# Kernel optimization log

Measured on AMD Instinct MI355X. Metric: run time of the kernel, lower is better.

The kernel has to match this reference:

```python
import jax, jax.numpy as jnp
import numpy as np

N = 50000      # nodes
E = 200000     # edges (before self-loops)
HID = 64       # hidden_channels
HEADS = 8
VOCAB = 100    # node-type vocabulary for the embedding
NEG_SLOPE = 0.2
EPS = 1e-16


def _gatv2(x, src, dst, Wl, bl, Wr, br, att, bias, heads, out_ch):
    """GATv2Conv (PyG defaults: share_weights=False, concat=True, neg_slope=0.2).
    x: [N, F_in]; src/dst: [E_tot] (self-loops already appended).
    Returns [N, heads*out_ch]."""
    n = x.shape[0]
    xl = (x @ Wl + bl).reshape(n, heads, out_ch)   # source transform
    xr = (x @ Wr + br).reshape(n, heads, out_ch)   # target transform
    m = xl[src] + xr[dst]                          # [E, H, C]
    e = jnp.einsum('ehc,hc->eh', jax.nn.leaky_relu(m, NEG_SLOPE), att)  # [E, H]
    # segment softmax over incoming edges of each destination node
    e_max = jax.ops.segment_max(e, dst, num_segments=n)
    e_exp = jnp.exp(e - e_max[dst])
    denom = jax.ops.segment_sum(e_exp, dst, num_segments=n)
    alpha = e_exp / (denom[dst] + EPS)             # [E, H]
    out = jax.ops.segment_sum(alpha[:, :, None] * xl[src], dst, num_segments=n)
    return out.reshape(n, heads * out_ch) + bias


def setup_inputs() -> dict:
    key = jax.random.key(0)
    ks = jax.random.split(key, 16)
    s = 0.1
    return {
        'x': jax.random.randint(ks[0], (N,), 0, VOCAB),
        'edge_index': jax.random.randint(ks[1], (2, E), 0, N),
        'emb': jax.random.normal(ks[2], (VOCAB, HID), dtype=jnp.float32) * s,
        'Wl1': jax.random.normal(ks[3], (HID, HEADS * HID), dtype=jnp.float32) * s,
        'bl1': jnp.zeros((HEADS * HID,), jnp.float32),
        'Wr1': jax.random.normal(ks[4], (HID, HEADS * HID), dtype=jnp.float32) * s,
        'br1': jnp.zeros((HEADS * HID,), jnp.float32),
        'att1': jax.random.normal(ks[5], (HEADS, HID), dtype=jnp.float32) * s,
        'bias1': jnp.zeros((HEADS * HID,), jnp.float32),
        'Wl2': jax.random.normal(ks[6], (HEADS * HID, 2), dtype=jnp.float32) * s,
        'bl2': jnp.zeros((2,), jnp.float32),
        'Wr2': jax.random.normal(ks[7], (HEADS * HID, 2), dtype=jnp.float32) * s,
        'br2': jnp.zeros((2,), jnp.float32),
        'att2': jax.random.normal(ks[8], (1, 2), dtype=jnp.float32) * s,
        'bias2': jnp.zeros((2,), jnp.float32),
    }


def reference(x, edge_index, emb, Wl1, bl1, Wr1, br1, att1, bias1,
              Wl2, bl2, Wr2, br2, att2, bias2):
    # PyG GATv2Conv adds self-loops by default
    loops = jnp.arange(N, dtype=edge_index.dtype)
    src = jnp.concatenate([edge_index[0], loops])
    dst = jnp.concatenate([edge_index[1], loops])

    h = emb[x]                                       # embedding lookup [N, HID]
    # dropout layers are identity in eval mode
    h = _gatv2(h, src, dst, Wl1, bl1, Wr1, br1, att1, bias1, HEADS, HID)
    h = jax.nn.elu(h)
    out = _gatv2(h, src, dst, Wl2, bl2, Wr2, br2, att2, bias2, 1, 2)
    return out                                       # [N, 2]
```

## Files before the change

kernel.cpp:

```cpp
#include <hip/hip_runtime.h>
#include <hip/hip_fp16.h>
#include <math.h>

#define NEG_SLOPE 0.2f
#define EPSV 1e-16f
#define CAP 32
#define MAXV 100
#define NBLK 256

struct __align__(16) h8v { __half2 a, b, c, d; };

__global__ __launch_bounds__(256) void kA_tables_fill(
    const float* __restrict__ emb, const float* __restrict__ Wl1,
    const float* __restrict__ bl1, const float* __restrict__ Wr1,
    const float* __restrict__ br1,
    const int* __restrict__ srcE, const int* __restrict__ dstE,
    const int* __restrict__ x,
    float* __restrict__ table_l, float* __restrict__ table_r,
    __half* __restrict__ table_lh,
    int* __restrict__ cnt, int* __restrict__ adj,
    int nb_tab, int nb_E, int E, int N, int VOCAB, int tshift)
{
    int b = blockIdx.x;
    if (b < nb_tab) {
        int idx = b * 256 + threadIdx.x;
        if (idx < VOCAB * 512) {
            int t = idx >> 9, o = idx & 511;
            float sl = bl1[o], sr = br1[o];
            const float* e = emb + t * 64;
            #pragma unroll 8
            for (int k = 0; k < 64; ++k) {
                float ev = e[k];
                sl = fmaf(ev, Wl1[k * 512 + o], sl);
                sr = fmaf(ev, Wr1[k * 512 + o], sr);
            }
            table_l[idx] = sl;
            table_r[idx] = sr;
            table_lh[idx] = __float2half_rn(sl);
        }
    } else if (b < nb_tab + nb_E) {
        int e = (b - nb_tab) * 256 + threadIdx.x;
        if (e < E) {
            int d = dstE[e];
            int sv = srcE[e];
            int pos = 1 + atomicAdd(&cnt[d], 1);
            if (pos < CAP) adj[d * CAP + pos] = (sv << tshift) | x[sv];
        }
    } else {
        int d = (b - nb_tab - nb_E) * 256 + threadIdx.x;
        if (d < N) adj[d * CAP] = (d << tshift) | x[d];
    }
}

__global__ __launch_bounds__(256) void kB_epair(
    const float* __restrict__ table_l, const float* __restrict__ table_r,
    const float* __restrict__ att1, float* __restrict__ exp_pair, int VOCAB)
{
    int idx = blockIdx.x * 256 + threadIdx.x;
    if (idx >= VOCAB * VOCAB * 8) return;
    int h = idx & 7;
    int p = idx >> 3;
    int ts = p % VOCAB;
    int td = p / VOCAB;
    const float4* tl = (const float4*)(table_l + ts * 512 + h * 64);
    const float4* tr = (const float4*)(table_r + td * 512 + h * 64);
    const float4* a  = (const float4*)(att1 + h * 64);
    float s = 0.f;
    #pragma unroll
    for (int c4 = 0; c4 < 16; ++c4) {
        float4 l = tl[c4], r = tr[c4], av = a[c4];
        float m0 = l.x + r.x; m0 = m0 > 0.f ? m0 : NEG_SLOPE * m0; s = fmaf(m0, av.x, s);
        float m1 = l.y + r.y; m1 = m1 > 0.f ? m1 : NEG_SLOPE * m1; s = fmaf(m1, av.y, s);
        float m2 = l.z + r.z; m2 = m2 > 0.f ? m2 : NEG_SLOPE * m2; s = fmaf(m2, av.z, s);
        float m3 = l.w + r.w; m3 = m3 > 0.f ? m3 : NEG_SLOPE * m3; s = fmaf(m3, av.w, s);
    }
    exp_pair[idx] = __expf(s);
}

__global__ __launch_bounds__(1024, 1) void k4_node_agg(
    const int* __restrict__ x, const int* __restrict__ cnt,
    const int* __restrict__ adj,
    const __half* __restrict__ table_lh, const float* __restrict__ exp_pair,
    const float* __restrict__ bias1,
    const float* __restrict__ Wl2, const float* __restrict__ bl2,
    const float* __restrict__ Wr2, const float* __restrict__ br2,
    float2* __restrict__ xl2, float2* __restrict__ xr2,
    int N, int VOCAB, int tmask)
{
    __shared__ __half tab[MAXV * 512];
    int vcap = min(VOCAB, MAXV);
    {
        const int4* sp = (const int4*)table_lh;
        int4* tp = (int4*)tab;
        for (int i = threadIdx.x; i < vcap * 64; i += 1024) tp[i] = sp[i];
    }
    __syncthreads();

    int lane = threadIdx.x & 63;
    int wv = threadIdx.x >> 6;
    int hc = lane >> 3;

    int chunk = (N + (int)gridDim.x - 1) / (int)gridDim.x;
    int nd1 = min((int)(blockIdx.x + 1) * chunk, N);

    const float4* b4 = (const float4*)(bias1 + lane * 8);
    float4 b0 = b4[0], b1 = b4[1];
    float bb[8] = {b0.x, b0.y, b0.z, b0.w, b1.x, b1.y, b1.z, b1.w};
    const float4* wl4 = (const float4*)(Wl2 + lane * 16);
    const float4* wr4 = (const float4*)(Wr2 + lane * 16);

    for (int d0 = blockIdx.x * chunk + wv; d0 < nd1; d0 += 16) {
        int wid = __builtin_amdgcn_readfirstlane(d0);
        const int* arow = adj + wid * CAP;
        int4 A0 = ((const int4*)arow)[0];
        int4 A1 = ((const int4*)arow)[1];
        int deg = min(cnt[wid], CAP - 1) + 1;
        int td = x[wid];
        const float* ep = exp_pair + (size_t)td * (VOCAB * 8);

        int ts[8];
        ts[0] = A0.x & tmask; ts[1] = A0.y & tmask;
        ts[2] = A0.z & tmask; ts[3] = A0.w & tmask;
        ts[4] = A1.x & tmask; ts[5] = A1.y & tmask;
        ts[6] = A1.z & tmask; ts[7] = A1.w & tmask;
        #pragma unroll
        for (int e = 1; e < 8; ++e) if (e >= deg) ts[e] = ts[0];

        float sw = 0.f;
        float acc[8] = {0.f, 0.f, 0.f, 0.f, 0.f, 0.f, 0.f, 0.f};

        {
            float we[4];
            #pragma unroll
            for (int e = 0; e < 4; ++e) we[e] = ep[ts[e] * 8 + hc];
            h8v hv[4];
            #pragma unroll
            for (int e = 0; e < 4; ++e)
                hv[e] = *(const h8v*)(tab + ts[e] * 512 + lane * 8);
            #pragma unroll
            for (int e = 0; e < 4; ++e) {
                float w = (e < deg) ? we[e] : 0.f;
                sw += w;
                float2 p0 = __half22float2(hv[e].a);
                float2 p1 = __half22float2(hv[e].b);
                float2 p2 = __half22float2(hv[e].c);
                float2 p3 = __half22float2(hv[e].d);
                acc[0] = fmaf(w, p0.x, acc[0]); acc[1] = fmaf(w, p0.y, acc[1]);
                acc[2] = fmaf(w, p1.x, acc[2]); acc[3] = fmaf(w, p1.y, acc[3]);
                acc[4] = fmaf(w, p2.x, acc[4]); acc[5] = fmaf(w, p2.y, acc[5]);
                acc[6] = fmaf(w, p3.x, acc[6]); acc[7] = fmaf(w, p3.y, acc[7]);
            }
        }
        if (deg > 4) {
            float we[4];
            #pragma unroll
            for (int e = 0; e < 4; ++e) we[e] = ep[ts[4 + e] * 8 + hc];
            h8v hv[4];
            #pragma unroll
            for (int e = 0; e < 4; ++e)
                hv[e] = *(const h8v*)(tab + ts[4 + e] * 512 + lane * 8);
            #pragma unroll
            for (int e = 0; e < 4; ++e) {
                float w = (4 + e < deg) ? we[e] : 0.f;
                sw += w;
                float2 p0 = __half22float2(hv[e].a);
                float2 p1 = __half22float2(hv[e].b);
                float2 p2 = __half22float2(hv[e].c);
                float2 p3 = __half22float2(hv[e].d);
                acc[0] = fmaf(w, p0.x, acc[0]); acc[1] = fmaf(w, p0.y, acc[1]);
                acc[2] = fmaf(w, p1.x, acc[2]); acc[3] = fmaf(w, p1.y, acc[3]);
                acc[4] = fmaf(w, p2.x, acc[4]); acc[5] = fmaf(w, p2.y, acc[5]);
                acc[6] = fmaf(w, p3.x, acc[6]); acc[7] = fmaf(w, p3.y, acc[7]);
            }
        }
        if (deg > 8) {
            for (int base = 8; base < deg; base += 4) {
                int t4i[4];
                #pragma unroll
                for (int u = 0; u < 4; ++u) {
                    int e = base + u;
                    t4i[u] = ((e < deg) ? arow[e] : arow[0]) & tmask;
                }
                float w4[4];
                #pragma unroll
                for (int u = 0; u < 4; ++u) w4[u] = ep[t4i[u] * 8 + hc];
                h8v g4[4];
                #pragma unroll
                for (int u = 0; u < 4; ++u)
                    g4[u] = *(const h8v*)(tab + t4i[u] * 512 + lane * 8);
                #pragma unroll
                for (int u = 0; u < 4; ++u) {
                    float w = (base + u < deg) ? w4[u] : 0.f;
                    sw += w;
                    float2 p0 = __half22float2(g4[u].a);
                    float2 p1 = __half22float2(g4[u].b);
                    float2 p2 = __half22float2(g4[u].c);
                    float2 p3 = __half22float2(g4[u].d);
                    acc[0] = fmaf(w, p0.x, acc[0]); acc[1] = fmaf(w, p0.y, acc[1]);
                    acc[2] = fmaf(w, p1.x, acc[2]); acc[3] = fmaf(w, p1.y, acc[3]);
                    acc[4] = fmaf(w, p2.x, acc[4]); acc[5] = fmaf(w, p2.y, acc[5]);
                    acc[6] = fmaf(w, p3.x, acc[6]); acc[7] = fmaf(w, p3.y, acc[7]);
                }
            }
        }
        float inv_dn = 1.f / (sw + EPSV);

        float h1[8];
        #pragma unroll
        for (int j = 0; j < 8; ++j) {
            float v = fmaf(acc[j], inv_dn, bb[j]);
            h1[j] = v > 0.f ? v : (__expf(v) - 1.f);
        }
        float sl0 = 0.f, sl1 = 0.f, sr0 = 0.f, sr1 = 0.f;
        #pragma unroll
        for (int k = 0; k < 4; ++k) {
            float4 vl = wl4[k], vr = wr4[k];
            float ha = h1[2 * k], hb = h1[2 * k + 1];
            sl0 = fmaf(ha, vl.x, sl0); sl1 = fmaf(ha, vl.y, sl1);
            sl0 = fmaf(hb, vl.z, sl0); sl1 = fmaf(hb, vl.w, sl1);
            sr0 = fmaf(ha, vr.x, sr0); sr1 = fmaf(ha, vr.y, sr1);
            sr0 = fmaf(hb, vr.z, sr0); sr1 = fmaf(hb, vr.w, sr1);
        }
        #pragma unroll
        for (int mm = 1; mm < 64; mm <<= 1) {
            sl0 += __shfl_xor(sl0, mm);
            sl1 += __shfl_xor(sl1, mm);
            sr0 += __shfl_xor(sr0, mm);
            sr1 += __shfl_xor(sr1, mm);
        }
        if (lane == 0) {
            xl2[wid] = make_float2(sl0 + bl2[0], sl1 + bl2[1]);
            xr2[wid] = make_float2(sr0 + br2[0], sr1 + br2[1]);
        }
    }
}

__global__ __launch_bounds__(256) void k5_layer2(
    const int* __restrict__ cnt, const int* __restrict__ adj,
    const float2* __restrict__ xl2, const float2* __restrict__ xr2,
    const float* __restrict__ att2, const float* __restrict__ bias2,
    float2* __restrict__ out, int N, int tshift)
{
    int wid = blockIdx.x * 4 + (threadIdx.x >> 6);
    int lane = threadIdx.x & 63;
    int g = lane >> 3, j = lane & 7;
    int d = wid * 8 + g;
    int dc = min(d, N - 1);
    int start = dc * CAP;
    float a0 = att2[0], a1 = att2[1];

    int aw = adj[start + j];
    int deg = min(cnt[dc], CAP - 1) + 1;
    float2 xr = xr2[dc];
    int src = min(aw >> tshift, N - 1);
    float2 xl = xl2[src];
    float m0 = xl.x + xr.x; m0 = m0 > 0.f ? m0 : NEG_SLOPE * m0;
    float m1 = xl.y + xr.y; m1 = m1 > 0.f ? m1 : NEG_SLOPE * m1;
    float ev = fmaf(a0, m0, a1 * m1);
    float w = (j < deg) ? __expf(ev) : 0.f;
    float s = w, o0 = w * xl.x, o1 = w * xl.y;

    for (int e = j + 8; e < deg; e += 8) {
        int src2 = min(adj[start + e] >> tshift, N - 1);
        float2 x2 = xl2[src2];
        float n0 = x2.x + xr.x; n0 = n0 > 0.f ? n0 : NEG_SLOPE * n0;
        float n1 = x2.y + xr.y; n1 = n1 > 0.f ? n1 : NEG_SLOPE * n1;
        float e2 = fmaf(a0, n0, a1 * n1);
        float w2 = __expf(e2);
        s += w2;
        o0 = fmaf(w2, x2.x, o0);
        o1 = fmaf(w2, x2.y, o1);
    }
    #pragma unroll
    for (int off = 1; off < 8; off <<= 1) {
        s  += __shfl_xor(s, off);
        o0 += __shfl_xor(o0, off);
        o1 += __shfl_xor(o1, off);
    }
    if (d < N && j == 0) {
        float inv = 1.f / (s + EPSV);
        out[d] = make_float2(fmaf(o0, inv, bias2[0]), fmaf(o1, inv, bias2[1]));
    }
}

extern "C" void kernel_launch(void* const* d_in, const int* in_sizes, int n_in,
                              void* d_out, int out_size, void* d_ws, size_t ws_size,
                              hipStream_t stream) {
    (void)n_in; (void)out_size; (void)ws_size;
    const int*   x     = (const int*)d_in[0];
    const int*   ei    = (const int*)d_in[1];
    const float* emb   = (const float*)d_in[2];
    const float* Wl1   = (const float*)d_in[3];
    const float* bl1   = (const float*)d_in[4];
    const float* Wr1   = (const float*)d_in[5];
    const float* br1   = (const float*)d_in[6];
    const float* att1  = (const float*)d_in[7];
    const float* bias1 = (const float*)d_in[8];
    const float* Wl2   = (const float*)d_in[9];
    const float* bl2   = (const float*)d_in[10];
    const float* Wr2   = (const float*)d_in[11];
    const float* br2   = (const float*)d_in[12];
    const float* att2  = (const float*)d_in[13];
    const float* bias2 = (const float*)d_in[14];
    float* out = (float*)d_out;

    int N = in_sizes[0];
    int E = in_sizes[1] / 2;
    int VOCAB = in_sizes[2] / 64;
    const int* srcE = ei;
    const int* dstE = ei + E;

    int tshift = 1;
    while ((1 << tshift) < VOCAB) ++tshift;
    int tmask = (1 << tshift) - 1;

    float*  table_l  = (float*)d_ws;
    float*  table_r  = table_l + (size_t)VOCAB * 512;
    float*  exp_pair = table_r + (size_t)VOCAB * 512;
    __half* table_lh = (__half*)(exp_pair + (size_t)VOCAB * VOCAB * 8);
    int*    cnt      = (int*)(table_lh + (size_t)VOCAB * 512);
    int*    adj      = cnt + ((N + 3) & ~3);
    float*  xl2      = (float*)(adj + (size_t)N * CAP);
    float*  xr2      = xl2 + 2 * (size_t)N;

    hipMemsetAsync(cnt, 0, sizeof(int) * (size_t)N, stream);

    int nb_tab = (VOCAB * 512 + 255) / 256;
    int nb_E = (E + 255) / 256;
    int nb_N = (N + 255) / 256;

    kA_tables_fill<<<nb_tab + nb_E + nb_N, 256, 0, stream>>>(
        emb, Wl1, bl1, Wr1, br1, srcE, dstE, x,
        table_l, table_r, table_lh, cnt, adj, nb_tab, nb_E, E, N, VOCAB, tshift);

    int nb_ep = (VOCAB * VOCAB * 8 + 255) / 256;
    kB_epair<<<nb_ep, 256, 0, stream>>>(table_l, table_r, att1, exp_pair, VOCAB);

    k4_node_agg<<<NBLK, 1024, 0, stream>>>(
        x, cnt, adj, table_lh, exp_pair, bias1, Wl2, bl2, Wr2, br2,
        (float2*)xl2, (float2*)xr2, N, VOCAB, tmask);

    k5_layer2<<<(N + 31) / 32, 256, 0, stream>>>(
        cnt, adj, (const float2*)xl2, (const float2*)xr2,
        att2, bias2, (float2*)out, N, tshift);
}
```

Baseline: 149.8 us.

## Prefetch per-destination exp row into LDS asynchronously and store exp pairs in fp16

The exp-pair table is now stored in half precision. Each wave copies the row for its destination type (800 halves) into a per-wave LDS buffer with global_load_lds. The copy for the next node is issued while the current node is still aggregating, and that node's adjacency and degree are also loaded one iteration ahead. Weight gathers come from LDS instead of scattered global reads, which hides gather latency. In exchange, shared memory use goes up, ordering relies on hand-placed waitcnt instructions, and the attention weights lose precision.

```diff
diff --git a/kernel.cpp b/kernel.cpp
--- a/kernel.cpp
+++ b/kernel.cpp
@@ -9,6 +9,12 @@
 #define NBLK 256
 
 struct __align__(16) h8v { __half2 a, b, c, d; };
+
+typedef __attribute__((address_space(1))) const unsigned int* gas1_t;
+typedef __attribute__((address_space(3))) unsigned int* las3_t;
+__device__ __forceinline__ void cp16_g2l(const void* g, void* l) {
+    __builtin_amdgcn_global_load_lds((gas1_t)g, (las3_t)l, 16, 0, 0);
+}
 
 __global__ __launch_bounds__(256) void kA_tables_fill(
     const float* __restrict__ emb, const float* __restrict__ Wl1,
@@ -54,7 +60,7 @@
 
 __global__ __launch_bounds__(256) void kB_epair(
     const float* __restrict__ table_l, const float* __restrict__ table_r,
-    const float* __restrict__ att1, float* __restrict__ exp_pair, int VOCAB)
+    const float* __restrict__ att1, __half* __restrict__ exph, int VOCAB)
 {
     int idx = blockIdx.x * 256 + threadIdx.x;
     if (idx >= VOCAB * VOCAB * 8) return;
@@ -74,13 +80,13 @@
         float m2 = l.z + r.z; m2 = m2 > 0.f ? m2 : NEG_SLOPE * m2; s = fmaf(m2, av.z, s);
         float m3 = l.w + r.w; m3 = m3 > 0.f ? m3 : NEG_SLOPE * m3; s = fmaf(m3, av.w, s);
     }
-    exp_pair[idx] = __expf(s);
+    exph[idx] = __float2half_rn(__expf(s));
 }
 
 __global__ __launch_bounds__(1024, 1) void k4_node_agg(
     const int* __restrict__ x, const int* __restrict__ cnt,
     const int* __restrict__ adj,
-    const __half* __restrict__ table_lh, const float* __restrict__ exp_pair,
+    const __half* __restrict__ table_lh, const __half* __restrict__ exph,
     const float* __restrict__ bias1,
     const float* __restrict__ Wl2, const float* __restrict__ bl2,
     const float* __restrict__ Wr2, const float* __restrict__ br2,
@@ -88,6 +94,7 @@
     int N, int VOCAB, int tmask)
 {
     __shared__ __half tab[MAXV * 512];
+    __shared__ __half eprow[16][800];
     int vcap = min(VOCAB, MAXV);
     {
         const int4* sp = (const int4*)table_lh;
@@ -100,23 +107,41 @@
     int wv = threadIdx.x >> 6;
     int hc = lane >> 3;
 
-    int chunk = (N + (int)gridDim.x - 1) / (int)gridDim.x;
-    int nd1 = min((int)(blockIdx.x + 1) * chunk, N);
-
-    const float4* b4 = (const float4*)(bias1 + lane * 8);
-    float4 b0 = b4[0], b1 = b4[1];
-    float bb[8] = {b0.x, b0.y, b0.z, b0.w, b1.x, b1.y, b1.z, b1.w};
+    int chunk = (N + NBLK - 1) / NBLK;
+    int b0 = blockIdx.x * chunk;
+    int nd1 = min(b0 + chunk, N);
+    int d0 = b0 + wv;
+    if (d0 >= nd1) return;
+
+    const float4* bp4 = (const float4*)(bias1 + lane * 8);
+    float4 bv0 = bp4[0], bv1 = bp4[1];
+    float bb[8] = {bv0.x, bv0.y, bv0.z, bv0.w, bv1.x, bv1.y, bv1.z, bv1.w};
     const float4* wl4 = (const float4*)(Wl2 + lane * 16);
     const float4* wr4 = (const float4*)(Wr2 + lane * 16);
 
-    for (int d0 = blockIdx.x * chunk + wv; d0 < nd1; d0 += 16) {
-        int wid = __builtin_amdgcn_readfirstlane(d0);
-        const int* arow = adj + wid * CAP;
-        int4 A0 = ((const int4*)arow)[0];
-        int4 A1 = ((const int4*)arow)[1];
-        int deg = min(cnt[wid], CAP - 1) + 1;
-        int td = x[wid];
-        const float* ep = exp_pair + (size_t)td * (VOCAB * 8);
+    __half* myrow = &eprow[wv][0];
+    const char* glane1 = (const char*)nullptr;
+
+    int tdC = x[d0];
+    {
+        const char* g = (const char*)(exph + (size_t)tdC * (VOCAB * 8));
+        cp16_g2l(g + lane * 16, (void*)myrow);
+        if (lane < 36)
+            cp16_g2l(g + 1024 + lane * 16, (void*)((char*)myrow + 1024));
+    }
+    int dn_seed = d0 + 16; if (dn_seed >= nd1) dn_seed = d0;
+    int tdN = x[dn_seed];
+    const int* arC = adj + d0 * CAP;
+    int4 A0 = ((const int4*)arC)[0];
+    int4 A1 = ((const int4*)arC)[1];
+    int degC = min(cnt[d0], CAP - 1) + 1;
+
+    for (int d = d0; d < nd1; d += 16) {
+        int dnext = d + 16;
+        bool hasN = dnext < nd1;
+        int dn1 = hasN ? dnext : d;
+        int dn2 = d + 32; if (dn2 >= nd1) dn2 = dn1;
+        const int* arow = adj + d * CAP;
 
         int ts[8];
         ts[0] = A0.x & tmask; ts[1] = A0.y & tmask;
@@ -124,73 +149,43 @@
         ts[4] = A1.x & tmask; ts[5] = A1.y & tmask;
         ts[6] = A1.z & tmask; ts[7] = A1.w & tmask;
         #pragma unroll
-        for (int e = 1; e < 8; ++e) if (e >= deg) ts[e] = ts[0];
+        for (int e = 1; e < 8; ++e) if (e >= degC) ts[e] = ts[0];
+
+        asm volatile("s_waitcnt vmcnt(0)" ::: "memory");
+
+        float we[8];
+        #pragma unroll
+        for (int e = 0; e < 4; ++e) we[e] = __half2float(myrow[ts[e] * 8 + hc]);
+        if (degC > 4) {
+            #pragma unroll
+            for (int e = 4; e < 8; ++e) we[e] = __half2float(myrow[ts[e] * 8 + hc]);
+        } else {
+            #pragma unroll
+            for (int e = 4; e < 8; ++e) we[e] = 0.f;
+        }
 
         float sw = 0.f;
         float acc[8] = {0.f, 0.f, 0.f, 0.f, 0.f, 0.f, 0.f, 0.f};
 
-        {
-            float we[4];
-            #pragma unroll
-            for (int e = 0; e < 4; ++e) we[e] = ep[ts[e] * 8 + hc];
-            h8v hv[4];
-            #pragma unroll
-            for (int e = 0; e < 4; ++e)
-                hv[e] = *(const h8v*)(tab + ts[e] * 512 + lane * 8);
-            #pragma unroll
-            for (int e = 0; e < 4; ++e) {
-                float w = (e < deg) ? we[e] : 0.f;
-                sw += w;
-                float2 p0 = __half22float2(hv[e].a);
-                float2 p1 = __half22float2(hv[e].b);
-                float2 p2 = __half22float2(hv[e].c);
-                float2 p3 = __half22float2(hv[e].d);
-                acc[0] = fmaf(w, p0.x, acc[0]); acc[1] = fmaf(w, p0.y, acc[1]);
-                acc[2] = fmaf(w, p1.x, acc[2]); acc[3] = fmaf(w, p1.y, acc[3]);
-                acc[4] = fmaf(w, p2.x, acc[4]); acc[5] = fmaf(w, p2.y, acc[5]);
-                acc[6] = fmaf(w, p3.x, acc[6]); acc[7] = fmaf(w, p3.y, acc[7]);
-            }
-        }
-        if (deg > 4) {
-            float we[4];
-            #pragma unroll
-            for (int e = 0; e < 4; ++e) we[e] = ep[ts[4 + e] * 8 + hc];
-            h8v hv[4];
-            #pragma unroll
-            for (int e = 0; e < 4; ++e)
-                hv[e] = *(const h8v*)(tab + ts[4 + e] * 512 + lane * 8);
-            #pragma unroll
-            for (int e = 0; e < 4; ++e) {
-                float w = (4 + e < deg) ? we[e] : 0.f;
-                sw += w;
-                float2 p0 = __half22float2(hv[e].a);
-                float2 p1 = __half22float2(hv[e].b);
-                float2 p2 = __half22float2(hv[e].c);
-                float2 p3 = __half22float2(hv[e].d);
-                acc[0] = fmaf(w, p0.x, acc[0]); acc[1] = fmaf(w, p0.y, acc[1]);
-                acc[2] = fmaf(w, p1.x, acc[2]); acc[3] = fmaf(w, p1.y, acc[3]);
-                acc[4] = fmaf(w, p2.x, acc[4]); acc[5] = fmaf(w, p2.y, acc[5]);
-                acc[6] = fmaf(w, p3.x, acc[6]); acc[7] = fmaf(w, p3.y, acc[7]);
-            }
-        }
-        if (deg > 8) {
-            for (int base = 8; base < deg; base += 4) {
+        if (degC > 8) {
+            for (int base = 8; base < degC; base += 4) {
                 int t4i[4];
                 #pragma unroll
                 for (int u = 0; u < 4; ++u) {
                     int e = base + u;
-                    t4i[u] = ((e < deg) ? arow[e] : arow[0]) & tmask;
+                    t4i[u] = ((e < degC) ? arow[e] : arow[0]) & tmask;
                 }
                 float w4[4];
                 #pragma unroll
-                for (int u = 0; u < 4; ++u) w4[u] = ep[t4i[u] * 8 + hc];
+                for (int u = 0; u < 4; ++u)
+                    w4[u] = __half2float(myrow[t4i[u] * 8 + hc]);
                 h8v g4[4];
                 #pragma unroll
                 for (int u = 0; u < 4; ++u)
                     g4[u] = *(const h8v*)(tab + t4i[u] * 512 + lane * 8);
                 #pragma unroll
                 for (int u = 0; u < 4; ++u) {
-                    float w = (base + u < deg) ? w4[u] : 0.f;
+                    float w = (base + u < degC) ? w4[u] : 0.f;
                     sw += w;
                     float2 p0 = __half22float2(g4[u].a);
                     float2 p1 = __half22float2(g4[u].b);
@@ -203,6 +198,61 @@
                 }
             }
         }
+
+        asm volatile("s_waitcnt lgkmcnt(0)" ::: "memory");
+        __builtin_amdgcn_sched_barrier(0);
+
+        {
+            const char* g = (const char*)(exph + (size_t)tdN * (VOCAB * 8));
+            cp16_g2l(g + lane * 16, (void*)myrow);
+            if (lane < 36)
+                cp16_g2l(g + 1024 + lane * 16, (void*)((char*)myrow + 1024));
+        }
+        int tdN_new = x[dn2];
+        const int* arN = adj + dn1 * CAP;
+        int4 A0N = ((const int4*)arN)[0];
+        int4 A1N = ((const int4*)arN)[1];
+        int degN = min(cnt[dn1], CAP - 1) + 1;
+
+        {
+            h8v hv[4];
+            #pragma unroll
+            for (int e = 0; e < 4; ++e)
+                hv[e] = *(const h8v*)(tab + ts[e] * 512 + lane * 8);
+            #pragma unroll
+            for (int e = 0; e < 4; ++e) {
+                float w = (e < degC) ? we[e] : 0.f;
+                sw += w;
+                float2 p0 = __half22float2(hv[e].a);
+                float2 p1 = __half22float2(hv[e].b);
+                float2 p2 = __half22float2(hv[e].c);
+                float2 p3 = __half22float2(hv[e].d);
+                acc[0] = fmaf(w, p0.x, acc[0]); acc[1] = fmaf(w, p0.y, acc[1]);
+                acc[2] = fmaf(w, p1.x, acc[2]); acc[3] = fmaf(w, p1.y, acc[3]);
+                acc[4] = fmaf(w, p2.x, acc[4]); acc[5] = fmaf(w, p2.y, acc[5]);
+                acc[6] = fmaf(w, p3.x, acc[6]); acc[7] = fmaf(w, p3.y, acc[7]);
+            }
+        }
+        if (degC > 4) {
+            h8v hv[4];
+            #pragma unroll
+            for (int e = 0; e < 4; ++e)
+                hv[e] = *(const h8v*)(tab + ts[4 + e] * 512 + lane * 8);
+            #pragma unroll
+            for (int e = 0; e < 4; ++e) {
+                float w = (4 + e < degC) ? we[4 + e] : 0.f;
+                sw += w;
+                float2 p0 = __half22float2(hv[e].a);
+                float2 p1 = __half22float2(hv[e].b);
+                float2 p2 = __half22float2(hv[e].c);
+                float2 p3 = __half22float2(hv[e].d);
+                acc[0] = fmaf(w, p0.x, acc[0]); acc[1] = fmaf(w, p0.y, acc[1]);
+                acc[2] = fmaf(w, p1.x, acc[2]); acc[3] = fmaf(w, p1.y, acc[3]);
+                acc[4] = fmaf(w, p2.x, acc[4]); acc[5] = fmaf(w, p2.y, acc[5]);
+                acc[6] = fmaf(w, p3.x, acc[6]); acc[7] = fmaf(w, p3.y, acc[7]);
+            }
+        }
+
         float inv_dn = 1.f / (sw + EPSV);
 
         float h1[8];
@@ -229,10 +279,13 @@
             sr1 += __shfl_xor(sr1, mm);
         }
         if (lane == 0) {
-            xl2[wid] = make_float2(sl0 + bl2[0], sl1 + bl2[1]);
-            xr2[wid] = make_float2(sr0 + br2[0], sr1 + br2[1]);
-        }
-    }
+            xl2[d] = make_float2(sl0 + bl2[0], sl1 + bl2[1]);
+            xr2[d] = make_float2(sr0 + br2[0], sr1 + br2[1]);
+        }
+
+        A0 = A0N; A1 = A1N; degC = degN; tdN = tdN_new;
+    }
+    (void)glane1;
 }
 
 __global__ __launch_bounds__(256) void k5_layer2(
@@ -316,9 +369,9 @@
 
     float*  table_l  = (float*)d_ws;
     float*  table_r  = table_l + (size_t)VOCAB * 512;
-    float*  exp_pair = table_r + (size_t)VOCAB * 512;
-    __half* table_lh = (__half*)(exp_pair + (size_t)VOCAB * VOCAB * 8);
-    int*    cnt      = (int*)(table_lh + (size_t)VOCAB * 512);
+    __half* table_lh = (__half*)(table_r + (size_t)VOCAB * 512);
+    __half* exph     = table_lh + (size_t)VOCAB * 512;
+    int*    cnt      = (int*)(exph + (size_t)VOCAB * VOCAB * 8);
     int*    adj      = cnt + ((N + 3) & ~3);
     float*  xl2      = (float*)(adj + (size_t)N * CAP);
     float*  xr2      = xl2 + 2 * (size_t)N;
@@ -334,10 +387,10 @@
         table_l, table_r, table_lh, cnt, adj, nb_tab, nb_E, E, N, VOCAB, tshift);
 
     int nb_ep = (VOCAB * VOCAB * 8 + 255) / 256;
-    kB_epair<<<nb_ep, 256, 0, stream>>>(table_l, table_r, att1, exp_pair, VOCAB);
+    kB_epair<<<nb_ep, 256, 0, stream>>>(table_l, table_r, att1, exph, VOCAB);
 
     k4_node_agg<<<NBLK, 1024, 0, stream>>>(
-        x, cnt, adj, table_lh, exp_pair, bias1, Wl2, bl2, Wr2, br2,
+        x, cnt, adj, table_lh, exph, bias1, Wl2, bl2, Wr2, br2,
         (float2*)xl2, (float2*)xr2, N, VOCAB, tmask);
 
     k5_layer2<<<(N + 31) / 32, 256, 0, stream>>>(
```

After: 156.0 us. +4.1%, slower.
